# Optimization experiments

Hardware: AMD Instinct MI355X
Metric: run time of the kernel (lower is better)

The kernel has to match this reference:

```python
import jax, jax.numpy as jnp
import numpy as np

WS = 14
NUM_HEADS = 12


def setup_inputs() -> dict:
    key = jax.random.key(0)
    ks = jax.random.split(key, 5)
    B, H, W, C = 16, 56, 56, 768
    x = jax.random.normal(ks[0], (B, H, W, C), dtype=jnp.float32)
    qkv_w = jax.random.normal(ks[1], (3 * C, C), dtype=jnp.float32) * (C ** -0.5)
    qkv_b = jax.random.normal(ks[2], (3 * C,), dtype=jnp.float32) * 0.02
    proj_w = jax.random.normal(ks[3], (C, C), dtype=jnp.float32) * (C ** -0.5)
    proj_b = jax.random.normal(ks[4], (C,), dtype=jnp.float32) * 0.02
    return {"x": x, "qkv_w": qkv_w, "qkv_b": qkv_b, "proj_w": proj_w, "proj_b": proj_b}


def reference(x, qkv_w, qkv_b, proj_w, proj_b):
    B, H, W, C = x.shape
    ws = WS
    h = NUM_HEADS
    hd = C // h
    scale = hd ** -0.5
    N = ws * ws
    # window partition: (B,H,W,C) -> (B*nw, ws*ws, C)
    xw = x.reshape(B, H // ws, ws, W // ws, ws, C)
    xw = xw.transpose(0, 1, 3, 2, 4, 5).reshape(-1, N, C)
    # qkv projection
    qkv = xw @ qkv_w.T + qkv_b                     # (nwB, N, 3C)
    qkv = qkv.reshape(-1, N, 3, h, hd)
    q, k, v = qkv[:, :, 0], qkv[:, :, 1], qkv[:, :, 2]   # (nwB, N, h, hd)
    attn = jnp.einsum('bnhd,bmhd->bhnm', q, k) * scale   # (nwB, h, N, N)
    attn = jax.nn.softmax(attn, axis=-1)
    o = jnp.einsum('bhnm,bmhd->bnhd', attn, v).reshape(-1, N, C)
    o = o @ proj_w.T + proj_b
    # window unpartition: (B*nw, ws, ws, C) -> (B, H, W, C)
    o = o.reshape(B, H // ws, W // ws, ws, ws, C)
    o = o.transpose(0, 1, 3, 2, 4, 5).reshape(B, H, W, C)
    return o
```

## Files before the change

### kernel.cpp

```cpp
#include <hip/hip_runtime.h>

typedef _Float16 half8 __attribute__((ext_vector_type(8)));
typedef _Float16 half4 __attribute__((ext_vector_type(4)));
typedef float f32x4 __attribute__((ext_vector_type(4)));

#define NTOK 196
#define NHEAD 12

__device__ __forceinline__ ushort f2h_u(float f) {
    _Float16 h = (_Float16)f;
    return __builtin_bit_cast(ushort, h);
}

__device__ __forceinline__ void gl_lds16(const ushort* g, ushort* l) {
    __builtin_amdgcn_global_load_lds((const __attribute__((address_space(1))) void*)g,
                                     (__attribute__((address_space(3))) void*)l,
                                     16, 0, 0);
}

__global__ __launch_bounds__(256) void cvt_x(const float* __restrict__ x,
                                             ushort* __restrict__ xb) {
    int idx = blockIdx.x * 256 + threadIdx.x;
    int t   = idx / 192;
    int c   = (idx - t * 192) * 4;
    int win = t / NTOK;
    int n   = t - win * NTOK;
    int b  = win >> 4, wh = (win >> 2) & 3, ww = win & 3;
    int r  = n / 14,  cc = n - r * 14;
    const float4 v = *(const float4*)(x + (((b * 56 + wh * 14 + r) * 56) + ww * 14 + cc) * 768 + c);
    ushort4 o = make_ushort4(f2h_u(v.x), f2h_u(v.y), f2h_u(v.z), f2h_u(v.w));
    *(ushort4*)(xb + t * 768 + c) = o;
}

__global__ __launch_bounds__(256) void cvt_w(const float* __restrict__ qkv_w,
                                             const float* __restrict__ proj_w,
                                             ushort* __restrict__ wq,
                                             ushort* __restrict__ wp) {
    int idx = blockIdx.x * 256 + threadIdx.x;
    int row = idx / 192;
    int c   = (idx - row * 192) * 4;
    const float* src;
    ushort* dst;
    if (row < 2304) { src = qkv_w + row * 768 + c;          dst = wq + row * 768 + c; }
    else            { src = proj_w + (row - 2304) * 768 + c; dst = wp + (row - 2304) * 768 + c; }
    float4 v = *(const float4*)src;
    *(ushort4*)dst = make_ushort4(f2h_u(v.x), f2h_u(v.y), f2h_u(v.z), f2h_u(v.w));
}

__device__ __forceinline__ void kloop256(const ushort* __restrict__ Ab,
                                         const ushort* __restrict__ Bb,
                                         ushort* sh,
                                         f32x4 (&acc)[8][4]) {
    const int tid = threadIdx.x, wave = tid >> 6, lane = tid & 63;
    const int quad = lane >> 4, l16 = lane & 15;
    const int wm = wave >> 2, wn = wave & 3;
    const int sr = lane >> 3;
    const int sc = ((lane & 7) ^ sr) * 8;
    const int rd_xor = (l16 & 7) << 4;
    const int rowB0 = (wn & 1) * 64;
    half8 Ar[4][2], Br[2][2][2];

#define STAGE_Q(srcK, ldsHalf, q) \
    gl_lds16((srcK) + ((q) * 64 + wave * 8 + sr) * 768 + sc, \
             (ldsHalf) + (((q) & 1) * 64 + wave * 8) * 64)

#define LD_A(QM, aB) \
    _Pragma("unroll") for (int mi = 0; mi < 4; ++mi) \
    _Pragma("unroll") for (int kk = 0; kk < 2; ++kk) \
        Ar[mi][kk] = *(const half8*)((aB) + \
            (((((QM) * 64 + mi * 16 + l16) * 128) + kk * 64 + quad * 16) ^ rd_xor))

#define LD_B(QN, bB) \
    _Pragma("unroll") for (int nj = 0; nj < 2; ++nj) \
    _Pragma("unroll") for (int kk = 0; kk < 2; ++kk) \
        Br[QN][nj][kk] = *(const half8*)((bB) + \
            ((((rowB0 + (QN) * 32 + nj * 16 + l16) * 128) + kk * 64 + quad * 16) ^ rd_xor))

#define MFMA_Q(QM, QN) \
    _Pragma("unroll") for (int mi = 0; mi < 4; ++mi) \
    _Pragma("unroll") for (int nj = 0; nj < 2; ++nj) \
    _Pragma("unroll") for (int kk = 0; kk < 2; ++kk) \
        acc[(QM) * 4 + mi][(QN) * 2 + nj] = __builtin_amdgcn_mfma_f32_16x16x32_f16( \
            Ar[mi][kk], Br[QN][nj][kk], acc[(QM) * 4 + mi][(QN) * 2 + nj], 0, 0, 0)

#define PH_SYNC_PRE() do { \
    __builtin_amdgcn_s_barrier(); \
    asm volatile("s_waitcnt lgkmcnt(0)" ::: "memory"); \
    __builtin_amdgcn_sched_barrier(0); \
    __builtin_amdgcn_s_setprio(1); } while (0)

#define PH_SYNC_POST() do { \
    __builtin_amdgcn_s_setprio(0); \
    __builtin_amdgcn_sched_barrier(0); \
    __builtin_amdgcn_s_barrier(); } while (0)

    {
        ushort* a0 = sh;
        ushort* b0 = sh + 32768;
        #pragma unroll
        for (int q = 0; q < 4; ++q) STAGE_Q(Ab, a0 + (q >> 1) * 8192, q);
        #pragma unroll
        for (int q = 0; q < 4; ++q) STAGE_Q(Bb, b0 + (q >> 1) * 8192, q);
        ushort* a1 = sh + 16384;
        ushort* b1 = sh + 32768 + 16384;
        STAGE_Q(Ab + 64, a1, 0);
        STAGE_Q(Ab + 64, a1 + 8192, 2);
        #pragma unroll
        for (int q = 0; q < 4; ++q) STAGE_Q(Bb + 64, b1 + (q >> 1) * 8192, q);
        asm volatile("s_waitcnt vmcnt(6)" ::: "memory");
        __builtin_amdgcn_s_barrier();
    }

    const int NT = 12;
    for (int T = 0; T < NT; ++T) {
        const int buf = T & 1;
        const char* aB = (const char*)(sh + buf * 16384 + wm * 8192);
        const char* bB = (const char*)(sh + 32768 + buf * 16384 + (wn >> 1) * 8192);
        ushort* aN = sh + (buf ^ 1) * 16384;
        ushort* aC = sh + buf * 16384;
        ushort* bC = sh + 32768 + buf * 16384;
        const bool p1 = (T + 1 < NT), p2 = (T + 2 < NT);

        LD_A(0, aB); LD_B(0, bB);
        if (p1) { STAGE_Q(Ab + (T + 1) * 64, aN, 1);
                  STAGE_Q(Ab + (T + 1) * 64, aN + 8192, 3); }
        PH_SYNC_PRE(); MFMA_Q(0, 0); PH_SYNC_POST();

        LD_B(1, bB);
        if (p2) { STAGE_Q(Ab + (T + 2) * 64, aC, 0);
                  STAGE_Q(Ab + (T + 2) * 64, aC + 8192, 2); }
        PH_SYNC_PRE(); MFMA_Q(0, 1); PH_SYNC_POST();

        LD_A(1, aB);
        if (p2) { STAGE_Q(Bb + (T + 2) * 64, bC, 0);
                  STAGE_Q(Bb + (T + 2) * 64, bC, 1); }
        PH_SYNC_PRE(); MFMA_Q(1, 1); PH_SYNC_POST();

        if (p2) { STAGE_Q(Bb + (T + 2) * 64, bC + 8192, 2);
                  STAGE_Q(Bb + (T + 2) * 64, bC + 8192, 3); }
        if (p2)      { asm volatile("s_waitcnt vmcnt(6)" ::: "memory"); }
        else if (p1) { asm volatile("s_waitcnt vmcnt(0)" ::: "memory"); }
        __builtin_amdgcn_s_barrier();
        __builtin_amdgcn_s_setprio(1);
        MFMA_Q(1, 0);
        __builtin_amdgcn_s_setprio(0);
        __builtin_amdgcn_sched_barrier(0);
        __builtin_amdgcn_s_barrier();
    }
#undef STAGE_Q
#undef LD_A
#undef LD_B
#undef MFMA_Q
#undef PH_SYNC_PRE
#undef PH_SYNC_POST
}

__global__ __launch_bounds__(512, 1) void gemm_qkv(const ushort* __restrict__ A,
                                                   const ushort* __restrict__ Wq,
                                                   const float* __restrict__ qkv_b,
                                                   ushort* __restrict__ qbuf,
                                                   ushort* __restrict__ kbuf,
                                                   ushort* __restrict__ vt,
                                                   int MB, int Wc) {
    __shared__ __align__(16) ushort sh[65536];
    const int tid = threadIdx.x, wave = tid >> 6, lane = tid & 63;
    const int quad = lane >> 4, l16 = lane & 15;
    const int wm = wave >> 2, wn = wave & 3;
    const int mblk = blockIdx.x % MB, nblk = blockIdx.x / MB;

    f32x4 acc[8][4];
    #pragma unroll
    for (int i = 0; i < 8; ++i)
        #pragma unroll
        for (int j = 0; j < 4; ++j) acc[i][j] = (f32x4){0.f, 0.f, 0.f, 0.f};

    kloop256(A + (size_t)mblk * 256 * 768, Wq + (size_t)nblk * 256 * 768, sh, acc);

    const int sec = nblk / 3;
    const int colq = nblk - sec * 3;
    #pragma unroll
    for (int nj = 0; nj < 4; ++nj) {
        const int col_in = colq * 256 + wn * 64 + nj * 16 + l16;
        const float bias = qkv_b[sec * 768 + col_in];
        #pragma unroll
        for (int mi = 0; mi < 8; ++mi) {
            #pragma unroll
            for (int r = 0; r < 4; ++r) {
                const int m = mblk * 256 + wm * 128 + mi * 16 + quad * 4 + r;
                const float v = acc[mi][nj][r] + bias;
                if (sec == 0) {
                    qbuf[(size_t)m * 768 + col_in] = f2h_u(v);
                } else if (sec == 1) {
                    kbuf[(size_t)m * 768 + col_in] = f2h_u(v);
                } else {
                    const int win = m / 196, tok = m - win * 196;
                    const int head = col_in >> 6, d = col_in & 63;
                    vt[((size_t)(head * Wc + win) * 64 + d) * 208 + tok] = f2h_u(v);
                }
            }
        }
    }
}

__global__ __launch_bounds__(256) void attn(const ushort* __restrict__ qbuf,
                                            const ushort* __restrict__ kbuf,
                                            const ushort* __restrict__ vt,
                                            ushort* __restrict__ ow, int Wc) {
    __shared__ __align__(16) ushort k_s[2 * 208 * 32];
    __shared__ __align__(16) ushort v_t[64 * 216];
    __shared__ __align__(16) ushort pscr[4 * 512];
    const int tid = threadIdx.x, wave = tid >> 6, lane = tid & 63;
    const int quad = lane >> 4, l16 = lane & 15;
    const int head = blockIdx.x % NHEAD, win = blockIdx.x / NHEAD;

    half8 aq0[4], aq1[4];
    #pragma unroll
    for (int si = 0; si < 4; ++si) {
        int strip = wave + si * 4; if (strip > 12) strip = 12;
        int qtok = strip * 16 + l16; if (qtok > 195) qtok = 195;
        const ushort* qp = qbuf + (size_t)(win * NTOK + qtok) * 768 + head * 64 + quad * 8;
        aq0[si] = *(const half8*)qp;
        aq1[si] = *(const half8*)(qp + 32);
    }

    for (int c = tid; c < 1664; c += 256) {
        const int row = c >> 3, c8 = c & 7;
        half8 val = {};
        if (row < NTOK)
            val = *(const half8*)(kbuf + (size_t)(win * NTOK + row) * 768 + head * 64 + c8 * 8);
        *(half8*)(k_s + ((c8 >> 2) * 208 + row) * 32 + (c8 & 3) * 8) = val;
    }
    {
        const ushort* vsrc = vt + (size_t)(head * Wc + win) * 64 * 208;
        for (int c = tid; c < 1664; c += 256) {
            const int d = c / 26, c8 = c - d * 26;
            *(half8*)(v_t + d * 216 + c8 * 8) = *(const half8*)(vsrc + d * 208 + c8 * 8);
        }
    }
    __syncthreads();

    ushort* ps = pscr + wave * 512;
    for (int si = 0; si < 4; ++si) {
        const int strip = wave + si * 4;
        if (strip > 12) break;
        f32x4 sacc[13];
        #pragma unroll
        for (int nt = 0; nt < 13; ++nt) sacc[nt] = (f32x4){0.f, 0.f, 0.f, 0.f};
        #pragma unroll
        for (int nt = 0; nt < 13; ++nt) {
            const int krow = (nt * 16 + l16) * 32 + quad * 8;
            half8 kb0 = *(const half8*)(k_s + krow);
            half8 kb1 = *(const half8*)(k_s + 208 * 32 + krow);
            sacc[nt] = __builtin_amdgcn_mfma_f32_16x16x32_f16(aq0[si], kb0, sacc[nt], 0, 0, 0);
            sacc[nt] = __builtin_amdgcn_mfma_f32_16x16x32_f16(aq1[si], kb1, sacc[nt], 0, 0, 0);
        }
        float P[13][4], linv[4];
        #pragma unroll
        for (int r = 0; r < 4; ++r) {
            float sv[13];
            float mx = -1e30f;
            #pragma unroll
            for (int nt = 0; nt < 13; ++nt) {
                float s = sacc[nt][r] * 0.125f;
                if (nt == 12 && l16 >= 4) s = -1e30f;
                sv[nt] = s;
                mx = fmaxf(mx, s);
            }
            mx = fmaxf(mx, __shfl_xor(mx, 1));
            mx = fmaxf(mx, __shfl_xor(mx, 2));
            mx = fmaxf(mx, __shfl_xor(mx, 4));
            mx = fmaxf(mx, __shfl_xor(mx, 8));
            float l = 0.f;
            #pragma unroll
            for (int nt = 0; nt < 13; ++nt) {
                float e = __expf(sv[nt] - mx);
                P[nt][r] = e;
                l += e;
            }
            l += __shfl_xor(l, 1);
            l += __shfl_xor(l, 2);
            l += __shfl_xor(l, 4);
            l += __shfl_xor(l, 8);
            linv[r] = 1.f / l;
        }
        f32x4 oacc[4];
        #pragma unroll
        for (int dt = 0; dt < 4; ++dt) oacc[dt] = (f32x4){0.f, 0.f, 0.f, 0.f};
        #pragma unroll
        for (int ks = 0; ks < 6; ++ks) {
            #pragma unroll
            for (int h = 0; h < 2; ++h) {
                const int nt = ks * 2 + h;
                #pragma unroll
                for (int r = 0; r < 4; ++r)
                    ps[(quad * 4 + r) * 32 + h * 16 + l16] = f2h_u(P[nt][r]);
            }
            half8 a = *(const half8*)(ps + l16 * 32 + quad * 8);
            #pragma unroll
            for (int dt = 0; dt < 4; ++dt) {
                half8 vb = *(const half8*)(v_t + (dt * 16 + l16) * 216 + ks * 32 + quad * 8);
                oacc[dt] = __builtin_amdgcn_mfma_f32_16x16x32_f16(a, vb, oacc[dt], 0, 0, 0);
            }
        }
        {
            #pragma unroll
            for (int r = 0; r < 4; ++r)
                ps[(quad * 4 + r) * 32 + l16] = f2h_u(P[12][r]);
            half4 a4 = *(const half4*)(ps + l16 * 32 + quad * 4);
            #pragma unroll
            for (int dt = 0; dt < 4; ++dt) {
                half4 vb4 = *(const half4*)(v_t + (dt * 16 + l16) * 216 + 192 + quad * 4);
                oacc[dt] = __builtin_amdgcn_mfma_f32_16x16x16f16(a4, vb4, oacc[dt], 0, 0, 0);
            }
        }
        const int sb = strip * 16;
        #pragma unroll
        for (int r = 0; r < 4; ++r) {
            const int token = sb + quad * 4 + r;
            if (token < NTOK) {
                #pragma unroll
                for (int dt = 0; dt < 4; ++dt)
                    ow[(size_t)(win * NTOK + token) * 768 + head * 64 + dt * 16 + l16] =
                        f2h_u(oacc[dt][r] * linv[r]);
            }
        }
    }
}

__global__ __launch_bounds__(512, 1) void proj_k(const ushort* __restrict__ ow,
                                                 const ushort* __restrict__ wp,
                                                 const float* __restrict__ pb,
                                                 float* __restrict__ out) {
    __shared__ __align__(16) ushort sh[65536];
    const int tid = threadIdx.x, wave = tid >> 6, lane = tid & 63;
    const int quad = lane >> 4, l16 = lane & 15;
    const int wm = wave >> 2, wn = wave & 3;
    const int mblk = blockIdx.x % 196, nblk = blockIdx.x / 196;

    f32x4 acc[8][4];
    #pragma unroll
    for (int i = 0; i < 8; ++i)
        #pragma unroll
        for (int j = 0; j < 4; ++j) acc[i][j] = (f32x4){0.f, 0.f, 0.f, 0.f};

    kloop256(ow + (size_t)mblk * 256 * 768, wp + (size_t)nblk * 256 * 768, sh, acc);

    #pragma unroll
    for (int mi = 0; mi < 8; ++mi) {
        #pragma unroll
        for (int r = 0; r < 4; ++r) {
            int grow = mblk * 256 + wm * 128 + mi * 16 + quad * 4 + r;
            int wnd = grow / 196, tok = grow - wnd * 196;
            int b = wnd >> 4, wh = (wnd >> 2) & 3, ww = wnd & 3;
            int rr = tok / 14, cc = tok - rr * 14;
            float* orow = out + ((b * 56 + wh * 14 + rr) * 56 + ww * 14 + cc) * 768;
            #pragma unroll
            for (int nj = 0; nj < 4; ++nj) {
                int col = nblk * 256 + wn * 64 + nj * 16 + l16;
                orow[col] = acc[mi][nj][r] + pb[col];
            }
        }
    }
}

extern "C" void kernel_launch(void* const* d_in, const int* in_sizes, int n_in,
                              void* d_out, int out_size, void* d_ws, size_t ws_size,
                              hipStream_t stream) {
    const float* x      = (const float*)d_in[0];
    const float* qkv_w  = (const float*)d_in[1];
    const float* qkv_b  = (const float*)d_in[2];
    const float* proj_w = (const float*)d_in[3];
    const float* proj_b = (const float*)d_in[4];
    float* out = (float*)d_out;

    char* ws = (char*)d_ws;
    ushort* xb = (ushort*)ws;
    ushort* wq = (ushort*)(ws + 77070336);
    ushort* wp = (ushort*)(ws + 80609280);
    char* dyn = ws + 81788928;

    size_t avail = ws_size > 81788928u ? ws_size - 81788928u : 0;
    int Wc = 256;
    while (Wc > 64 && (size_t)Wc * 921600u > avail) Wc >>= 1;
    const int nchunk = 256 / Wc;
    const int MB = Wc * NTOK / 256;

    ushort* qbuf = (ushort*)dyn;
    ushort* kbuf = qbuf + (size_t)Wc * NTOK * 768;
    ushort* vt   = kbuf + (size_t)Wc * NTOK * 768;

    cvt_x<<<37632, 256, 0, stream>>>(x, xb);
    cvt_w<<<2304, 256, 0, stream>>>(qkv_w, proj_w, wq, wp);
    hipMemsetAsync(vt, 0, (size_t)Wc * NHEAD * 64 * 208 * 2, stream);

    for (int c = 0; c < nchunk; ++c) {
        const ushort* xbc = xb + (size_t)c * Wc * NTOK * 768;
        ushort* owc = xb + (size_t)c * Wc * NTOK * 768;
        gemm_qkv<<<MB * 9, 512, 0, stream>>>(xbc, wq, qkv_b, qbuf, kbuf, vt, MB, Wc);
        attn<<<Wc * NHEAD, 256, 0, stream>>>(qbuf, kbuf, vt, owc, Wc);
    }
    proj_k<<<196 * 3, 512, 0, stream>>>(xb, wp, proj_b, out);
}
```

Baseline: 890.9 us.

## Swizzle GEMM blocks across XCDs and stage V transpose through LDS

Adds an XCD-aware block-index remap to the QKV and projection GEMMs, and reorders tiles so the N-blocks that share an M-block land together on one XCD and can reuse its L2. The V section of the QKV epilogue now transposes through shared memory, then writes 8-byte vectors of four consecutive tokens into the transposed V buffer. This replaces scattered 2-byte strided stores. The cost is extra barriers and LDS traffic in the V epilogue, and the 4-token groups assume windows align to multiples of 4 tokens (196 is divisible by 4).

```diff
diff --git a/kernel.cpp b/kernel.cpp
--- a/kernel.cpp
+++ b/kernel.cpp
@@ -16,6 +16,12 @@
     __builtin_amdgcn_global_load_lds((const __attribute__((address_space(1))) void*)g,
                                      (__attribute__((address_space(3))) void*)l,
                                      16, 0, 0);
+}
+
+__device__ __forceinline__ int xcd_swz(int bid, int nwg) {
+    const int x = bid & 7, o = bid >> 3;
+    const int qq = nwg >> 3, rr = nwg & 7;
+    return (x < rr ? x * (qq + 1) : rr * (qq + 1) + (x - rr) * qq) + o;
 }
 
 __global__ __launch_bounds__(256) void cvt_x(const float* __restrict__ x,
@@ -166,7 +172,8 @@
     const int tid = threadIdx.x, wave = tid >> 6, lane = tid & 63;
     const int quad = lane >> 4, l16 = lane & 15;
     const int wm = wave >> 2, wn = wave & 3;
-    const int mblk = blockIdx.x % MB, nblk = blockIdx.x / MB;
+    const int wg = xcd_swz(blockIdx.x, MB * 9);
+    const int mblk = wg / 9, nblk = wg - (wg / 9) * 9;
 
     f32x4 acc[8][4];
     #pragma unroll
@@ -178,25 +185,51 @@
 
     const int sec = nblk / 3;
     const int colq = nblk - sec * 3;
-    #pragma unroll
-    for (int nj = 0; nj < 4; ++nj) {
-        const int col_in = colq * 256 + wn * 64 + nj * 16 + l16;
-        const float bias = qkv_b[sec * 768 + col_in];
-        #pragma unroll
-        for (int mi = 0; mi < 8; ++mi) {
-            #pragma unroll
-            for (int r = 0; r < 4; ++r) {
-                const int m = mblk * 256 + wm * 128 + mi * 16 + quad * 4 + r;
-                const float v = acc[mi][nj][r] + bias;
-                if (sec == 0) {
-                    qbuf[(size_t)m * 768 + col_in] = f2h_u(v);
-                } else if (sec == 1) {
-                    kbuf[(size_t)m * 768 + col_in] = f2h_u(v);
-                } else {
-                    const int win = m / 196, tok = m - win * 196;
-                    const int head = col_in >> 6, d = col_in & 63;
-                    vt[((size_t)(head * Wc + win) * 64 + d) * 208 + tok] = f2h_u(v);
+    if (sec != 2) {
+        #pragma unroll
+        for (int nj = 0; nj < 4; ++nj) {
+            const int col_in = colq * 256 + wn * 64 + nj * 16 + l16;
+            const float bias = qkv_b[sec * 768 + col_in];
+            ushort* dst = (sec == 0) ? qbuf : kbuf;
+            #pragma unroll
+            for (int mi = 0; mi < 8; ++mi) {
+                #pragma unroll
+                for (int r = 0; r < 4; ++r) {
+                    const int m = mblk * 256 + wm * 128 + mi * 16 + quad * 4 + r;
+                    dst[(size_t)m * 768 + col_in] = f2h_u(acc[mi][nj][r] + bias);
                 }
+            }
+        }
+    } else {
+        const float* bv = qkv_b + 2 * 768;
+        #pragma unroll
+        for (int p = 0; p < 2; ++p) {
+            __syncthreads();
+            if (wm == p) {
+                #pragma unroll
+                for (int nj = 0; nj < 4; ++nj) {
+                    const int col = wn * 64 + nj * 16 + l16;
+                    const float bias = bv[colq * 256 + col];
+                    #pragma unroll
+                    for (int mi = 0; mi < 8; ++mi) {
+                        #pragma unroll
+                        for (int r = 0; r < 4; ++r)
+                            sh[col * 132 + mi * 16 + quad * 4 + r] =
+                                f2h_u(acc[mi][nj][r] + bias);
+                    }
+                }
+            }
+            __syncthreads();
+            #pragma unroll
+            for (int i = 0; i < 16; ++i) {
+                const int ch = i * 512 + tid;
+                const int col = ch >> 5, tq = ch & 31;
+                const int m = mblk * 256 + p * 128 + tq * 4;
+                const int win = m / 196, tok = m - win * 196;
+                const int cin = colq * 256 + col;
+                const int head = cin >> 6, d = cin & 63;
+                *(uint2*)(vt + ((size_t)(head * Wc + win) * 64 + d) * 208 + tok) =
+                    *(const uint2*)(sh + col * 132 + tq * 4);
             }
         }
     }
@@ -335,7 +368,8 @@
     const int tid = threadIdx.x, wave = tid >> 6, lane = tid & 63;
     const int quad = lane >> 4, l16 = lane & 15;
     const int wm = wave >> 2, wn = wave & 3;
-    const int mblk = blockIdx.x % 196, nblk = blockIdx.x / 196;
+    const int wg = xcd_swz(blockIdx.x, 196 * 3);
+    const int mblk = wg / 3, nblk = wg - (wg / 3) * 3;
 
     f32x4 acc[8][4];
     #pragma unroll
```

Measured after the change: 755.9 us. 1.18x faster.
